# Kernel tuning notes

Measured on AMD Instinct MI355X. Metric: run time of the kernel, lower is better.

Reference implementation:

```python
import jax, jax.numpy as jnp
import numpy as np

B, L, H, C = 1, 512, 1024, 2


def setup_inputs() -> dict:
    key = jax.random.key(0)
    k1, k2, k3 = jax.random.split(key, 3)
    lm_output = jax.random.normal(k1, (B, L, H), dtype=jnp.float32)
    # torch Linear weight layout: [out_features, in_features]
    W1 = jax.random.normal(k2, (H, 2 * H), dtype=jnp.float32) * 0.02
    b1 = jnp.zeros((H,), dtype=jnp.float32)
    W2 = jax.random.normal(k3, (C, H), dtype=jnp.float32) * 0.02
    b2 = jnp.zeros((C,), dtype=jnp.float32)
    return {"lm_output": lm_output, "W1": W1, "b1": b1, "W2": W2, "b2": b2}


def reference(lm_output, W1, b1, W2, b2):
    # pair_emb[b,i,j] = concat(lm_output[b,j], lm_output[b,i])
    # Linear(concat(a,b)) decomposes: split W1 into the halves acting on each part.
    Wa = W1[:, :H]  # acts on lm_output_a (the j / column token)
    Wb = W1[:, H:]  # acts on lm_output_b (the i / row token)
    a_proj = jnp.einsum('blh,oh->blo', lm_output, Wa)  # [B,L,H]
    b_proj = jnp.einsum('blh,oh->blo', lm_output, Wb)  # [B,L,H]
    # hidden[b,i,j] = tanh(a_proj[b,j] + b_proj[b,i] + b1)   -> [B,L,L,H]
    hidden = jnp.tanh(a_proj[:, None, :, :] + b_proj[:, :, None, :] + b1)
    # Dropout is identity at inference time.
    logits = jnp.einsum('bijh,ch->bijc', hidden, W2) + b2  # [B,L,L,C]
    logits = (logits + jnp.swapaxes(logits, 1, 2)) / 2.0
    return logits
```

## Files before the change

kernel.cpp:

```cpp
#include <hip/hip_runtime.h>

#define HH 1024
#define LL 512

typedef __attribute__((ext_vector_type(8))) short bf16x8;
typedef __attribute__((ext_vector_type(4))) float f32x4;

static __device__ __forceinline__ float fast_tanh(float x) {
    const float c = 2.8853900817779268f;
    const float e = __builtin_amdgcn_exp2f(c * x);
    const float r = __builtin_amdgcn_rcpf(e + 1.0f);
    return __builtin_fmaf(-2.0f, r, 1.0f);
}

static __device__ __forceinline__ ushort f2bf(float f) {
    unsigned u = __builtin_bit_cast(unsigned, f);
    u += 0x7fffu + ((u >> 16) & 1u);
    return (ushort)(u >> 16);
}

__global__ __launch_bounds__(256) void convert_kernel(
    const float* __restrict__ lm, const float* __restrict__ W1,
    ushort* __restrict__ lm16, ushort* __restrict__ B16)
{
    const int q = blockIdx.x * 256 + threadIdx.x;
    if (q < 131072) {
        const float4 v = ((const float4*)lm)[q];
        ushort4 o; o.x=f2bf(v.x); o.y=f2bf(v.y); o.z=f2bf(v.z); o.w=f2bf(v.w);
        ((ushort4*)lm16)[q] = o;
    } else {
        const int p = q - 131072;
        const int n = p >> 8, k4 = p & 255;
        const float4 v = *(const float4*)&W1[(n & 1023) * 2048 + (n >> 10) * 1024 + k4 * 4];
        ushort4 o; o.x=f2bf(v.x); o.y=f2bf(v.y); o.z=f2bf(v.z); o.w=f2bf(v.w);
        ((ushort4*)B16)[p] = o;
    }
}

__global__ __launch_bounds__(256) void proj_mfma_kernel(
    const ushort* __restrict__ lm16, const ushort* __restrict__ B16,
    const float* __restrict__ b1, float* __restrict__ Ta, float* __restrict__ Tb)
{
    __shared__ ushort As[32][72];
    __shared__ ushort Bs[64][72];

    const int tid  = threadIdx.x;
    const int lane = tid & 63;
    const int w    = tid >> 6;
    const int mbase = blockIdx.y * 32;
    const int nbase = blockIdx.x * 64;
    const int wm = (w & 1) * 16;
    const int wn = (w >> 1) * 32;

    f32x4 acc0 = {0.f, 0.f, 0.f, 0.f};
    f32x4 acc1 = {0.f, 0.f, 0.f, 0.f};

    const int srow = tid >> 3;
    const int sc8  = (tid & 7) * 8;

    const int mrow = lane & 15;
    const int q8   = (lane >> 4) * 8;

    for (int kb = 0; kb < HH; kb += 64) {
        __syncthreads();
        *(uint4*)&As[srow][sc8]      = *(const uint4*)&lm16[(mbase + srow) * HH + kb + sc8];
        *(uint4*)&Bs[srow][sc8]      = *(const uint4*)&B16[(nbase + srow) * HH + kb + sc8];
        *(uint4*)&Bs[srow + 32][sc8] = *(const uint4*)&B16[(nbase + srow + 32) * HH + kb + sc8];
        __syncthreads();

#pragma unroll
        for (int s = 0; s < 2; ++s) {
            const bf16x8 a  = *(const bf16x8*)&As[wm + mrow][s * 32 + q8];
            const bf16x8 b0 = *(const bf16x8*)&Bs[wn + mrow][s * 32 + q8];
            const bf16x8 b1f = *(const bf16x8*)&Bs[wn + 16 + mrow][s * 32 + q8];
            acc0 = __builtin_amdgcn_mfma_f32_16x16x32_bf16(a, b0, acc0, 0, 0, 0);
            acc1 = __builtin_amdgcn_mfma_f32_16x16x32_bf16(a, b1f, acc1, 0, 0, 0);
        }
    }

    const int col = lane & 15;
    const int rq  = (lane >> 4) * 4;
#pragma unroll
    for (int t = 0; t < 2; ++t) {
        const f32x4 acc = t ? acc1 : acc0;
        const int n_g = nbase + wn + t * 16 + col;
        const int m0  = mbase + wm + rq;
        if (n_g < HH) {
            const float bb = b1[n_g];
#pragma unroll
            for (int r = 0; r < 4; ++r)
                Ta[(m0 + r) * HH + n_g] = fast_tanh(acc[r] + bb);
        } else {
#pragma unroll
            for (int r = 0; r < 4; ++r)
                Tb[(m0 + r) * HH + (n_g - HH)] = fast_tanh(acc[r]);
        }
    }
}

__global__ __launch_bounds__(256) void pair_kernel(
    const float* __restrict__ Ta, const float* __restrict__ Tb,
    const float* __restrict__ W2, const float* __restrict__ b2,
    float* __restrict__ out)
{
    __shared__ float a_s[16][132];
    __shared__ float b_s[32][132];
    __shared__ float w0_s[HH], w1_s[HH];

    const int tid   = threadIdx.x;
    const int tx    = tid & 15;
    const int ty    = tid >> 4;
    const int jbase = blockIdx.x * 16;
    const int ibase = blockIdx.y * 32;

    {
        int p = tid;
#pragma unroll
        for (int it = 0; it < 2; ++it, p += 256) {
            const float4 v = ((const float4*)W2)[p];
            if (p < 256) ((float4*)w0_s)[p] = v;
            else         ((float4*)w1_s)[p - 256] = v;
        }
    }

    float acc00 = 0.f, acc01 = 0.f, acc10 = 0.f, acc11 = 0.f;

    for (int kb = 0; kb < HH; kb += 128) {
        __syncthreads();
        int p = tid;
#pragma unroll
        for (int it = 0; it < 6; ++it, p += 256) {
            const int row = p >> 5;
            const int c4  = p & 31;
            if (row < 16)
                *(float4*)&a_s[row][c4 * 4] = *(const float4*)&Ta[(jbase + row) * HH + kb + c4 * 4];
            else
                *(float4*)&b_s[row - 16][c4 * 4] = *(const float4*)&Tb[(ibase + row - 16) * HH + kb + c4 * 4];
        }
        __syncthreads();

#pragma unroll 8
        for (int h4 = 0; h4 < 32; ++h4) {
            const float4 ta4  = *(const float4*)&a_s[tx][h4 * 4];
            const float4 tb04 = *(const float4*)&b_s[ty][h4 * 4];
            const float4 tb14 = *(const float4*)&b_s[ty + 16][h4 * 4];
            const float4 w04  = *(const float4*)&w0_s[kb + h4 * 4];
            const float4 w14  = *(const float4*)&w1_s[kb + h4 * 4];

#define DO_H(TA, TB0, TB1, W0, W1V)                                  \
            {                                                        \
                const float n0 = (TA) + (TB0);                       \
                const float n1 = (TA) + (TB1);                       \
                const float d0 = __builtin_fmaf((TA), (TB0), 1.0f);  \
                const float d1 = __builtin_fmaf((TA), (TB1), 1.0f);  \
                const float r  = __builtin_amdgcn_rcpf(d0 * d1);     \
                const float t0 = n0 * (r * d1);                      \
                const float t1 = n1 * (r * d0);                      \
                acc00 = __builtin_fmaf(t0, (W0), acc00);             \
                acc01 = __builtin_fmaf(t0, (W1V), acc01);            \
                acc10 = __builtin_fmaf(t1, (W0), acc10);             \
                acc11 = __builtin_fmaf(t1, (W1V), acc11);            \
            }
            DO_H(ta4.x, tb04.x, tb14.x, w04.x, w14.x)
            DO_H(ta4.y, tb04.y, tb14.y, w04.y, w14.y)
            DO_H(ta4.z, tb04.z, tb14.z, w04.z, w14.z)
            DO_H(ta4.w, tb04.w, tb14.w, w04.w, w14.w)
#undef DO_H
        }
    }

    const float bb0 = b2[0];
    const float bb1 = b2[1];
    const int j  = jbase + tx;
    const int i0 = ibase + ty;
    const int i1 = ibase + ty + 16;
    float2* o2 = (float2*)out;
    o2[i0 * LL + j] = make_float2(acc00 + bb0, acc01 + bb1);
    o2[i1 * LL + j] = make_float2(acc10 + bb0, acc11 + bb1);
}

__global__ __launch_bounds__(256) void sym_kernel(float* __restrict__ out)
{
    const int idx = blockIdx.x * 256 + threadIdx.x;
    const int i = idx >> 9;
    const int j = idx & 511;
    if (j > i) {
        float2* o2 = (float2*)out;
        const float2 u = o2[i * LL + j];
        const float2 v = o2[j * LL + i];
        const float2 m = make_float2((u.x + v.x) * 0.5f, (u.y + v.y) * 0.5f);
        o2[i * LL + j] = m;
        o2[j * LL + i] = m;
    }
}

extern "C" void kernel_launch(void* const* d_in, const int* in_sizes, int n_in,
                              void* d_out, int out_size, void* d_ws, size_t ws_size,
                              hipStream_t stream)
{
    const float* lm = (const float*)d_in[0];
    const float* W1 = (const float*)d_in[1];
    const float* b1 = (const float*)d_in[2];
    const float* W2 = (const float*)d_in[3];
    const float* b2 = (const float*)d_in[4];
    float* out = (float*)d_out;

    ushort* lm16 = (ushort*)d_ws;
    ushort* B16  = (ushort*)((char*)d_ws + (size_t)(1 << 20));
    float*  Ta   = (float*) ((char*)d_ws + (size_t)(5 << 20));
    float*  Tb   = (float*) ((char*)d_ws + (size_t)(7 << 20));

    convert_kernel<<<2560, 256, 0, stream>>>(lm, W1, lm16, B16);
    proj_mfma_kernel<<<dim3(32, 16), 256, 0, stream>>>(lm16, B16, b1, Ta, Tb);
    pair_kernel<<<dim3(32, 16), 256, 0, stream>>>(Ta, Tb, W2, b2, out);
    sym_kernel<<<(LL * LL) / 256, 256, 0, stream>>>(out);
}
```

Baseline: 156.5 us.

## Use exp-form tanh, split-K pair kernel with atomic symmetric accumulation

Bf16 conversion of lm_output and W1 moves into the projection GEMM's tile loads, so the separate convert kernel is gone. The projection now stores exp(2x) instead of tanh. The pair kernel then rewrites tanh(a+b) as 1 - 2/(1+Ea·Eb), which lets one reciprocal serve a 2x2 register tile of pairs. The pair kernel also splits the hidden dimension four ways over blockIdx.z and atomically adds half-logits into both (i,j) and (j,i) of a zero-filled output, which replaces the separate symmetrization kernel. This trades large numbers of float atomics and a memset for less SFU work and fewer kernels, and exp values can overflow for large activations.

```diff
diff --git a/kernel.cpp b/kernel.cpp
--- a/kernel.cpp
+++ b/kernel.cpp
@@ -1,4 +1,5 @@
 #include <hip/hip_runtime.h>
+#include <hip/hip_bf16.h>
 
 #define HH 1024
 #define LL 512
@@ -6,40 +7,20 @@
 typedef __attribute__((ext_vector_type(8))) short bf16x8;
 typedef __attribute__((ext_vector_type(4))) float f32x4;
 
-static __device__ __forceinline__ float fast_tanh(float x) {
-    const float c = 2.8853900817779268f;
-    const float e = __builtin_amdgcn_exp2f(c * x);
-    const float r = __builtin_amdgcn_rcpf(e + 1.0f);
-    return __builtin_fmaf(-2.0f, r, 1.0f);
-}
-
-static __device__ __forceinline__ ushort f2bf(float f) {
-    unsigned u = __builtin_bit_cast(unsigned, f);
-    u += 0x7fffu + ((u >> 16) & 1u);
-    return (ushort)(u >> 16);
-}
-
-__global__ __launch_bounds__(256) void convert_kernel(
+static constexpr float C_EXP = 2.8853900817779268f;
+
+static __device__ __forceinline__ uint4 pack8(float4 a, float4 b) {
+    union { uint4 u; __hip_bfloat162 h[4]; } r;
+    r.h[0] = __float22bfloat162_rn(make_float2(a.x, a.y));
+    r.h[1] = __float22bfloat162_rn(make_float2(a.z, a.w));
+    r.h[2] = __float22bfloat162_rn(make_float2(b.x, b.y));
+    r.h[3] = __float22bfloat162_rn(make_float2(b.z, b.w));
+    return r.u;
+}
+
+__global__ __launch_bounds__(256) void proj_mfma_kernel(
     const float* __restrict__ lm, const float* __restrict__ W1,
-    ushort* __restrict__ lm16, ushort* __restrict__ B16)
-{
-    const int q = blockIdx.x * 256 + threadIdx.x;
-    if (q < 131072) {
-        const float4 v = ((const float4*)lm)[q];
-        ushort4 o; o.x=f2bf(v.x); o.y=f2bf(v.y); o.z=f2bf(v.z); o.w=f2bf(v.w);
-        ((ushort4*)lm16)[q] = o;
-    } else {
-        const int p = q - 131072;
-        const int n = p >> 8, k4 = p & 255;
-        const float4 v = *(const float4*)&W1[(n & 1023) * 2048 + (n >> 10) * 1024 + k4 * 4];
-        ushort4 o; o.x=f2bf(v.x); o.y=f2bf(v.y); o.z=f2bf(v.z); o.w=f2bf(v.w);
-        ((ushort4*)B16)[p] = o;
-    }
-}
-
-__global__ __launch_bounds__(256) void proj_mfma_kernel(
-    const ushort* __restrict__ lm16, const ushort* __restrict__ B16,
-    const float* __restrict__ b1, float* __restrict__ Ta, float* __restrict__ Tb)
+    const float* __restrict__ b1, float* __restrict__ Ea, float* __restrict__ Eb)
 {
     __shared__ ushort As[32][72];
     __shared__ ushort Bs[64][72];
@@ -52,6 +33,9 @@
     const int wm = (w & 1) * 16;
     const int wn = (w >> 1) * 32;
 
+    const int sel  = nbase >> 10;
+    const int nrow = nbase & 1023;
+
     f32x4 acc0 = {0.f, 0.f, 0.f, 0.f};
     f32x4 acc1 = {0.f, 0.f, 0.f, 0.f};
 
@@ -63,18 +47,23 @@
 
     for (int kb = 0; kb < HH; kb += 64) {
         __syncthreads();
-        *(uint4*)&As[srow][sc8]      = *(const uint4*)&lm16[(mbase + srow) * HH + kb + sc8];
-        *(uint4*)&Bs[srow][sc8]      = *(const uint4*)&B16[(nbase + srow) * HH + kb + sc8];
-        *(uint4*)&Bs[srow + 32][sc8] = *(const uint4*)&B16[(nbase + srow + 32) * HH + kb + sc8];
+        {
+            const float* pa = &lm[(mbase + srow) * HH + kb + sc8];
+            *(uint4*)&As[srow][sc8] = pack8(*(const float4*)pa, *(const float4*)(pa + 4));
+            const float* pb0 = &W1[(nrow + srow) * 2048 + sel * 1024 + kb + sc8];
+            *(uint4*)&Bs[srow][sc8] = pack8(*(const float4*)pb0, *(const float4*)(pb0 + 4));
+            const float* pb1 = &W1[(nrow + srow + 32) * 2048 + sel * 1024 + kb + sc8];
+            *(uint4*)&Bs[srow + 32][sc8] = pack8(*(const float4*)pb1, *(const float4*)(pb1 + 4));
+        }
         __syncthreads();
 
 #pragma unroll
         for (int s = 0; s < 2; ++s) {
             const bf16x8 a  = *(const bf16x8*)&As[wm + mrow][s * 32 + q8];
             const bf16x8 b0 = *(const bf16x8*)&Bs[wn + mrow][s * 32 + q8];
-            const bf16x8 b1f = *(const bf16x8*)&Bs[wn + 16 + mrow][s * 32 + q8];
+            const bf16x8 bf = *(const bf16x8*)&Bs[wn + 16 + mrow][s * 32 + q8];
             acc0 = __builtin_amdgcn_mfma_f32_16x16x32_bf16(a, b0, acc0, 0, 0, 0);
-            acc1 = __builtin_amdgcn_mfma_f32_16x16x32_bf16(a, b1f, acc1, 0, 0, 0);
+            acc1 = __builtin_amdgcn_mfma_f32_16x16x32_bf16(a, bf, acc1, 0, 0, 0);
         }
     }
 
@@ -89,108 +78,120 @@
             const float bb = b1[n_g];
 #pragma unroll
             for (int r = 0; r < 4; ++r)
-                Ta[(m0 + r) * HH + n_g] = fast_tanh(acc[r] + bb);
+                Ea[(m0 + r) * HH + n_g] = __builtin_amdgcn_exp2f(C_EXP * (acc[r] + bb));
         } else {
 #pragma unroll
             for (int r = 0; r < 4; ++r)
-                Tb[(m0 + r) * HH + (n_g - HH)] = fast_tanh(acc[r]);
-        }
-    }
-}
-
-__global__ __launch_bounds__(256) void pair_kernel(
-    const float* __restrict__ Ta, const float* __restrict__ Tb,
+                Eb[(m0 + r) * HH + (n_g - HH)] = __builtin_amdgcn_exp2f(C_EXP * acc[r]);
+        }
+    }
+}
+
+__global__ __launch_bounds__(256, 4) void pair_kernel(
+    const float* __restrict__ Ea, const float* __restrict__ Eb,
     const float* __restrict__ W2, const float* __restrict__ b2,
     float* __restrict__ out)
 {
-    __shared__ float a_s[16][132];
+    __shared__ float a_s[32][132];
     __shared__ float b_s[32][132];
-    __shared__ float w0_s[HH], w1_s[HH];
+    __shared__ float w0_s[256], w1_s[256];
+    __shared__ float s_red[2];
 
     const int tid   = threadIdx.x;
     const int tx    = tid & 15;
     const int ty    = tid >> 4;
-    const int jbase = blockIdx.x * 16;
+    const int jbase = blockIdx.x * 32;
     const int ibase = blockIdx.y * 32;
-
-    {
+    const int k0    = blockIdx.z * 256;
+
+    if (tid < 128) {
+        const int c = tid >> 6, q = tid & 63;
+        const float4 v = *(const float4*)&W2[c * HH + k0 + q * 4];
+        ((float4*)(c ? w1_s : w0_s))[q] =
+            make_float4(-2.f * v.x, -2.f * v.y, -2.f * v.z, -2.f * v.w);
+    }
+    if (tid < 128) {
+        const int c = tid >> 6, l = tid & 63;
+        const float* ws = c ? w1_s : w0_s;
+        float s = ws[l] + ws[l + 64] + ws[l + 128] + ws[l + 192];
+#pragma unroll
+        for (int off = 32; off; off >>= 1) s += __shfl_down(s, off, 64);
+        if (l == 0) s_red[c] = s;
+    }
+
+    float acc[2][2][2] = {};
+
+    for (int kb = 0; kb < 256; kb += 128) {
+        __syncthreads();
         int p = tid;
 #pragma unroll
-        for (int it = 0; it < 2; ++it, p += 256) {
-            const float4 v = ((const float4*)W2)[p];
-            if (p < 256) ((float4*)w0_s)[p] = v;
-            else         ((float4*)w1_s)[p - 256] = v;
-        }
-    }
-
-    float acc00 = 0.f, acc01 = 0.f, acc10 = 0.f, acc11 = 0.f;
-
-    for (int kb = 0; kb < HH; kb += 128) {
-        __syncthreads();
-        int p = tid;
-#pragma unroll
-        for (int it = 0; it < 6; ++it, p += 256) {
+        for (int it = 0; it < 8; ++it, p += 256) {
             const int row = p >> 5;
             const int c4  = p & 31;
-            if (row < 16)
-                *(float4*)&a_s[row][c4 * 4] = *(const float4*)&Ta[(jbase + row) * HH + kb + c4 * 4];
+            if (row < 32)
+                *(float4*)&a_s[row][c4 * 4] =
+                    *(const float4*)&Ea[(jbase + row) * HH + k0 + kb + c4 * 4];
             else
-                *(float4*)&b_s[row - 16][c4 * 4] = *(const float4*)&Tb[(ibase + row - 16) * HH + kb + c4 * 4];
-        }
-        __syncthreads();
-
-#pragma unroll 8
+                *(float4*)&b_s[row - 32][c4 * 4] =
+                    *(const float4*)&Eb[(ibase + row - 32) * HH + k0 + kb + c4 * 4];
+        }
+        __syncthreads();
+
+#pragma unroll 4
         for (int h4 = 0; h4 < 32; ++h4) {
-            const float4 ta4  = *(const float4*)&a_s[tx][h4 * 4];
-            const float4 tb04 = *(const float4*)&b_s[ty][h4 * 4];
-            const float4 tb14 = *(const float4*)&b_s[ty + 16][h4 * 4];
-            const float4 w04  = *(const float4*)&w0_s[kb + h4 * 4];
-            const float4 w14  = *(const float4*)&w1_s[kb + h4 * 4];
-
-#define DO_H(TA, TB0, TB1, W0, W1V)                                  \
-            {                                                        \
-                const float n0 = (TA) + (TB0);                       \
-                const float n1 = (TA) + (TB1);                       \
-                const float d0 = __builtin_fmaf((TA), (TB0), 1.0f);  \
-                const float d1 = __builtin_fmaf((TA), (TB1), 1.0f);  \
-                const float r  = __builtin_amdgcn_rcpf(d0 * d1);     \
-                const float t0 = n0 * (r * d1);                      \
-                const float t1 = n1 * (r * d0);                      \
-                acc00 = __builtin_fmaf(t0, (W0), acc00);             \
-                acc01 = __builtin_fmaf(t0, (W1V), acc01);            \
-                acc10 = __builtin_fmaf(t1, (W0), acc10);             \
-                acc11 = __builtin_fmaf(t1, (W1V), acc11);            \
+            const float4 ea0 = *(const float4*)&a_s[tx][h4 * 4];
+            const float4 ea1 = *(const float4*)&a_s[tx + 16][h4 * 4];
+            const float4 eb0 = *(const float4*)&b_s[ty][h4 * 4];
+            const float4 eb1 = *(const float4*)&b_s[ty + 16][h4 * 4];
+            const float4 w0  = *(const float4*)&w0_s[kb + h4 * 4];
+            const float4 w1  = *(const float4*)&w1_s[kb + h4 * 4];
+
+#define DO_H(EA0, EA1, EB0, EB1, W0V, W1V)                            \
+            {                                                         \
+                const float d00 = __builtin_fmaf((EB0), (EA0), 1.f);  \
+                const float d01 = __builtin_fmaf((EB0), (EA1), 1.f);  \
+                const float d10 = __builtin_fmaf((EB1), (EA0), 1.f);  \
+                const float d11 = __builtin_fmaf((EB1), (EA1), 1.f);  \
+                const float p0 = d00 * d01, p1 = d10 * d11;           \
+                const float R  = __builtin_amdgcn_rcpf(p0 * p1);      \
+                const float q0 = R * p1, q1 = R * p0;                 \
+                const float r00 = q0 * d01, r01 = q0 * d00;           \
+                const float r10 = q1 * d11, r11 = q1 * d10;           \
+                acc[0][0][0] = __builtin_fmaf(r00, (W0V), acc[0][0][0]); \
+                acc[0][0][1] = __builtin_fmaf(r00, (W1V), acc[0][0][1]); \
+                acc[0][1][0] = __builtin_fmaf(r01, (W0V), acc[0][1][0]); \
+                acc[0][1][1] = __builtin_fmaf(r01, (W1V), acc[0][1][1]); \
+                acc[1][0][0] = __builtin_fmaf(r10, (W0V), acc[1][0][0]); \
+                acc[1][0][1] = __builtin_fmaf(r10, (W1V), acc[1][0][1]); \
+                acc[1][1][0] = __builtin_fmaf(r11, (W0V), acc[1][1][0]); \
+                acc[1][1][1] = __builtin_fmaf(r11, (W1V), acc[1][1][1]); \
             }
-            DO_H(ta4.x, tb04.x, tb14.x, w04.x, w14.x)
-            DO_H(ta4.y, tb04.y, tb14.y, w04.y, w14.y)
-            DO_H(ta4.z, tb04.z, tb14.z, w04.z, w14.z)
-            DO_H(ta4.w, tb04.w, tb14.w, w04.w, w14.w)
+            DO_H(ea0.x, ea1.x, eb0.x, eb1.x, w0.x, w1.x)
+            DO_H(ea0.y, ea1.y, eb0.y, eb1.y, w0.y, w1.y)
+            DO_H(ea0.z, ea1.z, eb0.z, eb1.z, w0.z, w1.z)
+            DO_H(ea0.w, ea1.w, eb0.w, eb1.w, w0.w, w1.w)
 #undef DO_H
         }
     }
 
-    const float bb0 = b2[0];
-    const float bb1 = b2[1];
-    const int j  = jbase + tx;
-    const int i0 = ibase + ty;
-    const int i1 = ibase + ty + 16;
-    float2* o2 = (float2*)out;
-    o2[i0 * LL + j] = make_float2(acc00 + bb0, acc01 + bb1);
-    o2[i1 * LL + j] = make_float2(acc10 + bb0, acc11 + bb1);
-}
-
-__global__ __launch_bounds__(256) void sym_kernel(float* __restrict__ out)
-{
-    const int idx = blockIdx.x * 256 + threadIdx.x;
-    const int i = idx >> 9;
-    const int j = idx & 511;
-    if (j > i) {
-        float2* o2 = (float2*)out;
-        const float2 u = o2[i * LL + j];
-        const float2 v = o2[j * LL + i];
-        const float2 m = make_float2((u.x + v.x) * 0.5f, (u.y + v.y) * 0.5f);
-        o2[i * LL + j] = m;
-        o2[j * LL + i] = m;
+    const float sc0 = -0.25f * s_red[0];
+    const float sc1 = -0.25f * s_red[1];
+    const float bb0 = (blockIdx.z == 0) ? 0.5f * b2[0] : 0.f;
+    const float bb1 = (blockIdx.z == 0) ? 0.5f * b2[1] : 0.f;
+
+#pragma unroll
+    for (int ii = 0; ii < 2; ++ii) {
+#pragma unroll
+        for (int jj = 0; jj < 2; ++jj) {
+            const int i = ibase + ty + ii * 16;
+            const int j = jbase + tx + jj * 16;
+            const float v0 = 0.5f * acc[ii][jj][0] + sc0 + bb0;
+            const float v1 = 0.5f * acc[ii][jj][1] + sc1 + bb1;
+            atomicAdd(&out[(i * LL + j) * 2 + 0], v0);
+            atomicAdd(&out[(i * LL + j) * 2 + 1], v1);
+            atomicAdd(&out[(j * LL + i) * 2 + 0], v0);
+            atomicAdd(&out[(j * LL + i) * 2 + 1], v1);
+        }
     }
 }
 
@@ -205,13 +206,10 @@
     const float* b2 = (const float*)d_in[4];
     float* out = (float*)d_out;
 
-    ushort* lm16 = (ushort*)d_ws;
-    ushort* B16  = (ushort*)((char*)d_ws + (size_t)(1 << 20));
-    float*  Ta   = (float*) ((char*)d_ws + (size_t)(5 << 20));
-    float*  Tb   = (float*) ((char*)d_ws + (size_t)(7 << 20));
-
-    convert_kernel<<<2560, 256, 0, stream>>>(lm, W1, lm16, B16);
-    proj_mfma_kernel<<<dim3(32, 16), 256, 0, stream>>>(lm16, B16, b1, Ta, Tb);
-    pair_kernel<<<dim3(32, 16), 256, 0, stream>>>(Ta, Tb, W2, b2, out);
-    sym_kernel<<<(LL * LL) / 256, 256, 0, stream>>>(out);
-}
+    float* Ea = (float*)d_ws;
+    float* Eb = Ea + (size_t)LL * HH;
+
+    hipMemsetAsync(d_out, 0, (size_t)LL * LL * 2 * sizeof(float), stream);
+    proj_mfma_kernel<<<dim3(32, 16), 256, 0, stream>>>(lm, W1, b1, Ea, Eb);
+    pair_kernel<<<dim3(16, 16, 4), 256, 0, stream>>>(Ea, Eb, W2, b2, out);
+}
```

Measured after the change: 157.3 us. No clear change (+0.5%).
